# Optimization experiments

Measured on AMD Instinct MI355X. Metric: run time of the kernel, lower is better.

Reference implementation:

```python
import jax, jax.numpy as jnp
import numpy as np

P = 50000      # number of graph nodes (cortical dipoles)
HID = 256      # hidden width
E = 800000     # number of nonzeros in Ahat (avg degree 16)


def setup_inputs() -> dict:
    key = jax.random.key(0)
    ks = jax.random.split(key, 12)
    beta = jax.random.normal(ks[0], (P, 1), dtype=jnp.float32)
    degree = jax.random.uniform(ks[1], (P, 1), dtype=jnp.float32)
    A_rows = jax.random.randint(ks[2], (E,), 0, P, dtype=jnp.int32)
    A_cols = jax.random.randint(ks[3], (E,), 0, P, dtype=jnp.int32)
    # normalized-adjacency-like positive values
    A_vals = jax.random.uniform(ks[4], (E,), dtype=jnp.float32) * (1.0 / 16.0)
    # parameters (torch nn.Linear stores weight as [out, in])
    s_in = 1.0 / np.sqrt(3.0)
    s_h = 1.0 / np.sqrt(HID)
    W_in = jax.random.uniform(ks[5], (HID, 3), jnp.float32, -s_in, s_in)
    b_in = jax.random.uniform(ks[6], (HID,), jnp.float32, -s_in, s_in)
    W_mp1 = jax.random.uniform(ks[7], (HID, HID), jnp.float32, -s_h, s_h)
    W_mp2 = jax.random.uniform(ks[8], (HID, HID), jnp.float32, -s_h, s_h)
    W_out = jax.random.uniform(ks[9], (1, HID), jnp.float32, -s_h, s_h)
    b_out = jax.random.uniform(ks[10], (1,), jnp.float32, -s_h, s_h)
    return {
        "beta": beta, "degree": degree,
        "A_rows": A_rows, "A_cols": A_cols, "A_vals": A_vals,
        "W_in": W_in, "b_in": b_in,
        "W_mp1": W_mp1, "W_mp2": W_mp2,
        "W_out": W_out, "b_out": b_out,
    }


def _spmm(A_rows, A_cols, A_vals, X):
    # sparse [P,P] @ dense [P,H] via gather + segment-sum over COO edges
    msgs = A_vals[:, None] * X[A_cols]            # [E, H]
    return jax.ops.segment_sum(msgs, A_rows, num_segments=P)


def reference(beta, degree, A_rows, A_cols, A_vals,
              W_in, b_in, W_mp1, W_mp2, W_out, b_out):
    x = jnp.concatenate([beta, beta ** 2, degree], axis=1)   # [P, 3]
    h = jax.nn.relu(x @ W_in.T + b_in)                       # [P, HID]
    AH = _spmm(A_rows, A_cols, A_vals, h)                    # one-hop
    A2H = _spmm(A_rows, A_cols, A_vals, AH)                  # two-hop
    h = jax.nn.relu(AH @ W_mp1.T + A2H @ W_mp2.T)            # fused sum + relu
    g = jax.nn.softplus(h @ W_out.T + b_out)                 # [P, 1]
    return g
```

## Files before the change

kernel.cpp:

```cpp
#include <hip/hip_runtime.h>
#include <math.h>

#define NP 50000
#define HIDDEN 256
#define NE 800000
#define CAP 64

#define NSLICE 8
#define SLICE_ROWS 6250
#define BPS 256

#define OFF_AH     0ULL
#define OFF_A2H    25600000ULL
#define OFF_BP     51200000ULL
#define OFF_CNT    51462144ULL
#define OFF_PC     51662144ULL
#define OFF_EV     52062144ULL

typedef __attribute__((ext_vector_type(8))) short bf16x8;
typedef __attribute__((ext_vector_type(8))) unsigned short u16x8;
typedef __attribute__((ext_vector_type(4))) float f32x4;

__device__ inline unsigned short f2bf(float f) {
    union { float f; unsigned int u; } x; x.f = f;
    unsigned int r = x.u + 0x7FFFu + ((x.u >> 16) & 1u);
    return (unsigned short)(r >> 16);
}
__device__ inline float bf2f(unsigned short u) {
    union { unsigned int u; float f; } x; x.u = ((unsigned int)u) << 16; return x.f;
}

__global__ void bp_kernel(const float* __restrict__ W1,
                          const float* __restrict__ W2,
                          unsigned short* __restrict__ Bp) {
    int t = blockIdx.x * 256 + threadIdx.x;
    int j = t >> 9;
    int k = t & 511;
    float v = (k < 256) ? W1[j * 256 + k] : W2[j * 256 + (k - 256)];
    Bp[(k >> 3) * 2048 + j * 8 + (k & 7)] = f2bf(v);
}

__global__ void pc_kernel(const float* __restrict__ beta,
                          const float* __restrict__ degree,
                          float2* __restrict__ pc) {
    int i = blockIdx.x * 256 + threadIdx.x;
    if (i < NP) pc[i] = make_float2(beta[i], degree[i]);
}

__global__ __launch_bounds__(256) void scatter_sliced(
        const int* __restrict__ rows, const int* __restrict__ cols,
        const float* __restrict__ vals,
        int* __restrict__ cnt, int2* __restrict__ ev) {
    int slice = blockIdx.x & (NSLICE - 1);
    int bj = blockIdx.x >> 3;
    int rlo = slice * SLICE_ROWS;
    int rhi = rlo + SLICE_ROWS;
    for (int e = bj * 256 + threadIdx.x; e < NE; e += BPS * 256) {
        int r = rows[e];
        if (r >= rlo && r < rhi) {
            int pos = atomicAdd(&cnt[r], 1);
            if (pos < CAP)
                ev[(size_t)r * CAP + pos] = make_int2(cols[e], __float_as_int(vals[e]));
        }
    }
}

__global__ __launch_bounds__(256) void spmm_embed_kernel(
        const int* __restrict__ cnt, const int2* __restrict__ ev,
        const float2* __restrict__ pc,
        const float* __restrict__ W_in, const float* __restrict__ b_in,
        unsigned short* __restrict__ Y) {
    int w = threadIdx.x >> 6;
    int lane = threadIdx.x & 63;
    int r = blockIdx.x * 4 + w;
    if (r >= NP) return;
    int half = lane >> 5;
    int fo = (lane & 31) * 8;

    int n = min(cnt[r], CAP);
    int2 e2 = make_int2(0, 0);
    if (lane < n) e2 = ev[(size_t)r * CAP + lane];
    int col_l = e2.x;
    float val_l = __int_as_float(e2.y);

    float wr0[8], wr1[8], wr2[8], br[8];
    #pragma unroll
    for (int j = 0; j < 8; ++j) {
        wr0[j] = W_in[(fo + j) * 3 + 0];
        wr1[j] = W_in[(fo + j) * 3 + 1];
        wr2[j] = W_in[(fo + j) * 3 + 2];
        br[j]  = b_in[fo + j];
    }

    float acc[8] = {0.f,0.f,0.f,0.f,0.f,0.f,0.f,0.f};

#define ESTEP(d)                                                             \
    {                                                                        \
        float2 pr[d]; float vr[d];                                           \
        _Pragma("unroll")                                                    \
        for (int k = 0; k < (d); ++k) {                                      \
            int e = i + 2 * k + half;                                        \
            int c = __shfl(col_l, e);                                        \
            vr[k] = __shfl(val_l, e);                                        \
            pr[k] = pc[c];                                                   \
        }                                                                    \
        _Pragma("unroll")                                                    \
        for (int k = 0; k < (d); ++k) {                                      \
            float b = pr[k].x, dd = pr[k].y, v = vr[k];                      \
            float b2 = b * b;                                                \
            _Pragma("unroll")                                                \
            for (int j = 0; j < 8; ++j) {                                    \
                float t = fmaf(b, wr0[j], fmaf(b2, wr1[j], fmaf(dd, wr2[j], br[j]))); \
                acc[j] = fmaf(v, fmaxf(t, 0.f), acc[j]);                     \
            }                                                                \
        }                                                                    \
    }

    int i = 0;
    for (; i + 16 <= n; i += 16) ESTEP(8)
    if (i + 8 <= n) { ESTEP(4) i += 8; }
    if (i + 4 <= n) { ESTEP(2) i += 4; }
    if (i < n)      { ESTEP(2) }
#undef ESTEP

    #pragma unroll
    for (int j = 0; j < 8; ++j) acc[j] += __shfl_xor(acc[j], 32);
    if (half == 0) {
        u16x8 o;
        #pragma unroll
        for (int j = 0; j < 8; ++j) o[j] = f2bf(acc[j]);
        *reinterpret_cast<u16x8*>(Y + (size_t)r * HIDDEN + fo) = o;
    }
}

__global__ __launch_bounds__(256) void spmm_gather_kernel(
        const int* __restrict__ cnt, const int2* __restrict__ ev,
        const unsigned short* __restrict__ X,
        unsigned short* __restrict__ Y) {
    int w = threadIdx.x >> 6;
    int lane = threadIdx.x & 63;
    int r = blockIdx.x * 4 + w;
    if (r >= NP) return;
    int half = lane >> 5;
    int fo = (lane & 31) * 8;

    int n = min(cnt[r], CAP);
    int2 e2 = make_int2(0, 0);
    if (lane < n) e2 = ev[(size_t)r * CAP + lane];
    int col_l = e2.x;
    float val_l = __int_as_float(e2.y);

    float acc[8] = {0.f,0.f,0.f,0.f,0.f,0.f,0.f,0.f};

#define GSTEP(d)                                                             \
    {                                                                        \
        u16x8 xr[d]; float vr[d];                                            \
        _Pragma("unroll")                                                    \
        for (int k = 0; k < (d); ++k) {                                      \
            int e = i + 2 * k + half;                                        \
            int c = __shfl(col_l, e);                                        \
            vr[k] = __shfl(val_l, e);                                        \
            xr[k] = *reinterpret_cast<const u16x8*>(X + (size_t)c * HIDDEN + fo); \
        }                                                                    \
        _Pragma("unroll")                                                    \
        for (int k = 0; k < (d); ++k)                                        \
            _Pragma("unroll")                                                \
            for (int j = 0; j < 8; ++j)                                      \
                acc[j] = fmaf(vr[k], bf2f(xr[k][j]), acc[j]);                \
    }

    int i = 0;
    for (; i + 16 <= n; i += 16) GSTEP(8)
    if (i + 8 <= n) { GSTEP(4) i += 8; }
    if (i + 4 <= n) { GSTEP(2) i += 4; }
    if (i < n)      { GSTEP(2) }
#undef GSTEP

    #pragma unroll
    for (int j = 0; j < 8; ++j) acc[j] += __shfl_xor(acc[j], 32);
    if (half == 0) {
        u16x8 o;
        #pragma unroll
        for (int j = 0; j < 8; ++j) o[j] = f2bf(acc[j]);
        *reinterpret_cast<u16x8*>(Y + (size_t)r * HIDDEN + fo) = o;
    }
}

__global__ __launch_bounds__(512, 4) void mp_out_kernel(
        const unsigned short* __restrict__ AH,
        const unsigned short* __restrict__ A2H,
        const unsigned short* __restrict__ Bp,
        const float* __restrict__ W_out, const float* __restrict__ b_out,
        float* __restrict__ g) {
    __shared__ unsigned short As[128 * 64];
    __shared__ unsigned short Bs[8 * 256 * 8];
    __shared__ float Ps[4][128];

    int tid = threadIdx.x;
    int w = tid >> 6;
    int lane = tid & 63;
    int wr = w >> 2;
    int wc = w & 3;
    int p0 = blockIdx.x * 128;

    f32x4 acc[4][4];
    #pragma unroll
    for (int i = 0; i < 4; ++i)
        #pragma unroll
        for (int j = 0; j < 4; ++j)
            acc[i][j] = (f32x4){0.f, 0.f, 0.f, 0.f};

    for (int kc = 0; kc < 8; ++kc) {
        const unsigned short* Xsrc = (kc < 4) ? AH : A2H;
        int k0 = (kc & 3) * 64;
        __syncthreads();
        #pragma unroll
        for (int it = 0; it < 2; ++it) {
            int slot = it * 512 + tid;
            int ss = slot ^ ((slot >> 3) & 7);
            int row = ss >> 3;
            int ko = (ss & 7) * 8;
            int grow = p0 + row;
            if (grow >= NP) grow = NP - 1;
            float4 v = *reinterpret_cast<const float4*>(Xsrc + (size_t)grow * HIDDEN + k0 + ko);
            *reinterpret_cast<float4*>(&As[slot * 8]) = v;
        }
        #pragma unroll
        for (int it = 0; it < 4; ++it) {
            int c2 = it * 512 + tid;
            float4 v = *reinterpret_cast<const float4*>(
                Bp + ((size_t)(kc * 8 + (c2 >> 8))) * 2048 + (c2 & 255) * 8);
            *reinterpret_cast<float4*>(&Bs[c2 * 8]) = v;
        }
        __syncthreads();
        #pragma unroll
        for (int ks = 0; ks < 2; ++ks) {
            bf16x8 af[4], bfr[4];
            #pragma unroll
            for (int rt = 0; rt < 4; ++rt) {
                int row = wr * 64 + rt * 16 + (lane & 15);
                int elem = row * 64 + ks * 32 + (lane >> 4) * 8;
                elem ^= (row & 7) << 3;
                af[rt] = *reinterpret_cast<const bf16x8*>(&As[elem]);
            }
            #pragma unroll
            for (int nt = 0; nt < 4; ++nt) {
                int col = wc * 64 + nt * 16 + (lane & 15);
                int kbl = ks * 4 + (lane >> 4);
                bfr[nt] = *reinterpret_cast<const bf16x8*>(&Bs[kbl * 2048 + col * 8]);
            }
            #pragma unroll
            for (int rt = 0; rt < 4; ++rt)
                #pragma unroll
                for (int nt = 0; nt < 4; ++nt)
                    acc[rt][nt] = __builtin_amdgcn_mfma_f32_16x16x32_bf16(
                        af[rt], bfr[nt], acc[rt][nt], 0, 0, 0);
        }
    }

    float wv[4];
    #pragma unroll
    for (int nt = 0; nt < 4; ++nt)
        wv[nt] = W_out[wc * 64 + nt * 16 + (lane & 15)];

    float ps[4][4];
    #pragma unroll
    for (int rt = 0; rt < 4; ++rt)
        #pragma unroll
        for (int r = 0; r < 4; ++r) {
            float s = 0.f;
            #pragma unroll
            for (int nt = 0; nt < 4; ++nt)
                s = fmaf(fmaxf(acc[rt][nt][r], 0.0f), wv[nt], s);
            ps[rt][r] = s;
        }
    #pragma unroll
    for (int m = 1; m < 16; m <<= 1)
        #pragma unroll
        for (int rt = 0; rt < 4; ++rt)
            #pragma unroll
            for (int r = 0; r < 4; ++r)
                ps[rt][r] += __shfl_xor(ps[rt][r], m);

    if ((lane & 15) == 0) {
        int rb = wr * 64 + (lane >> 4) * 4;
        #pragma unroll
        for (int rt = 0; rt < 4; ++rt)
            #pragma unroll
            for (int r = 0; r < 4; ++r)
                Ps[wc][rb + rt * 16 + r] = ps[rt][r];
    }
    __syncthreads();
    if (tid < 128) {
        int p = p0 + tid;
        if (p < NP) {
            float z = Ps[0][tid] + Ps[1][tid] + Ps[2][tid] + Ps[3][tid] + b_out[0];
            g[p] = fmaxf(z, 0.0f) + log1pf(expf(-fabsf(z)));
        }
    }
}

extern "C" void kernel_launch(void* const* d_in, const int* in_sizes, int n_in,
                              void* d_out, int out_size, void* d_ws, size_t ws_size,
                              hipStream_t stream) {
    const float* beta   = (const float*)d_in[0];
    const float* degree = (const float*)d_in[1];
    const int*   A_rows = (const int*)d_in[2];
    const int*   A_cols = (const int*)d_in[3];
    const float* A_vals = (const float*)d_in[4];
    const float* W_in   = (const float*)d_in[5];
    const float* b_in   = (const float*)d_in[6];
    const float* W_mp1  = (const float*)d_in[7];
    const float* W_mp2  = (const float*)d_in[8];
    const float* W_out  = (const float*)d_in[9];
    const float* b_out  = (const float*)d_in[10];
    float* g = (float*)d_out;

    char* ws = (char*)d_ws;
    unsigned short* AH  = (unsigned short*)(ws + OFF_AH);
    unsigned short* A2H = (unsigned short*)(ws + OFF_A2H);
    unsigned short* Bp  = (unsigned short*)(ws + OFF_BP);
    int*    cnt = (int*)(ws + OFF_CNT);
    float2* pc  = (float2*)(ws + OFF_PC);
    int2*   ev  = (int2*)(ws + OFF_EV);

    hipMemsetAsync(cnt, 0, NP * sizeof(int), stream);

    bp_kernel<<<512, 256, 0, stream>>>(W_mp1, W_mp2, Bp);
    pc_kernel<<<(NP + 255) / 256, 256, 0, stream>>>(beta, degree, pc);

    scatter_sliced<<<NSLICE * BPS, 256, 0, stream>>>(A_rows, A_cols, A_vals, cnt, ev);

    spmm_embed_kernel<<<(NP + 3) / 4, 256, 0, stream>>>(cnt, ev, pc, W_in, b_in, AH);
    spmm_gather_kernel<<<(NP + 3) / 4, 256, 0, stream>>>(cnt, ev, AH, A2H);

    mp_out_kernel<<<(NP + 127) / 128, 512, 0, stream>>>(AH, A2H, Bp, W_out, b_out, g);
}
```

Before: 171.1 us.

## Use persistent waves with edge-list prefetch in SpMM kernels; fuse prep kernels

The two SpMM kernels become persistent: a grid of 2048 blocks whose waves loop over rows with a stride, prefetching the next row's count and edge list while the current row is processed. The variable-depth unrolled steps are replaced by a fixed 4-pair step plus one masked tail step. The weight repack, the beta/degree packing and the counter memset are merged into one prep kernel to cut launch overhead. In exchange, each wave holds fewer gathers in flight per step, which could reduce memory-level parallelism. The unmasked read of ev past the count also reads stale workspace entries, which are only consumed through masked lanes.

```diff
diff --git a/kernel.cpp b/kernel.cpp
--- a/kernel.cpp
+++ b/kernel.cpp
@@ -9,6 +9,9 @@
 #define NSLICE 8
 #define SLICE_ROWS 6250
 #define BPS 256
+
+#define PWB 2048
+#define PWAVES (PWB * 4)
 
 #define OFF_AH     0ULL
 #define OFF_A2H    25600000ULL
@@ -30,21 +33,27 @@
     union { unsigned int u; float f; } x; x.u = ((unsigned int)u) << 16; return x.f;
 }
 
-__global__ void bp_kernel(const float* __restrict__ W1,
-                          const float* __restrict__ W2,
-                          unsigned short* __restrict__ Bp) {
-    int t = blockIdx.x * 256 + threadIdx.x;
-    int j = t >> 9;
-    int k = t & 511;
-    float v = (k < 256) ? W1[j * 256 + k] : W2[j * 256 + (k - 256)];
-    Bp[(k >> 3) * 2048 + j * 8 + (k & 7)] = f2bf(v);
-}
-
-__global__ void pc_kernel(const float* __restrict__ beta,
-                          const float* __restrict__ degree,
-                          float2* __restrict__ pc) {
-    int i = blockIdx.x * 256 + threadIdx.x;
-    if (i < NP) pc[i] = make_float2(beta[i], degree[i]);
+__global__ void prep_kernel(const float* __restrict__ W1,
+                            const float* __restrict__ W2,
+                            unsigned short* __restrict__ Bp,
+                            const float* __restrict__ beta,
+                            const float* __restrict__ degree,
+                            float2* __restrict__ pc,
+                            int* __restrict__ cnt) {
+    int b = blockIdx.x;
+    if (b < 512) {
+        int t = b * 256 + threadIdx.x;
+        int j = t >> 9;
+        int k = t & 511;
+        float v = (k < 256) ? W1[j * 256 + k] : W2[j * 256 + (k - 256)];
+        Bp[(k >> 3) * 2048 + j * 8 + (k & 7)] = f2bf(v);
+    } else if (b < 708) {
+        int i = (b - 512) * 256 + threadIdx.x;
+        if (i < NP) pc[i] = make_float2(beta[i], degree[i]);
+    } else {
+        int i = (b - 708) * 256 + threadIdx.x;
+        if (i < NP) cnt[i] = 0;
+    }
 }
 
 __global__ __launch_bounds__(256) void scatter_sliced(
@@ -72,16 +81,8 @@
         unsigned short* __restrict__ Y) {
     int w = threadIdx.x >> 6;
     int lane = threadIdx.x & 63;
-    int r = blockIdx.x * 4 + w;
-    if (r >= NP) return;
     int half = lane >> 5;
     int fo = (lane & 31) * 8;
-
-    int n = min(cnt[r], CAP);
-    int2 e2 = make_int2(0, 0);
-    if (lane < n) e2 = ev[(size_t)r * CAP + lane];
-    int col_l = e2.x;
-    float val_l = __int_as_float(e2.y);
 
     float wr0[8], wr1[8], wr2[8], br[8];
     #pragma unroll
@@ -92,20 +93,40 @@
         br[j]  = b_in[fo + j];
     }
 
-    float acc[8] = {0.f,0.f,0.f,0.f,0.f,0.f,0.f,0.f};
-
-#define ESTEP(d)                                                             \
+    int r = blockIdx.x * 4 + w;
+    if (r >= NP) return;
+    int  n_cur = cnt[r];
+    int2 e_cur = ev[(size_t)r * CAP + lane];
+
+    while (true) {
+        int rn = r + PWAVES;
+        int  n_nxt = 0;
+        int2 e_nxt = make_int2(0, 0);
+        if (rn < NP) {
+            n_nxt = cnt[rn];
+            e_nxt = ev[(size_t)rn * CAP + lane];
+        }
+
+        int n = min(n_cur, CAP);
+        int col_l = e_cur.x;
+        float val_l = __int_as_float(e_cur.y);
+        float acc[8] = {0.f,0.f,0.f,0.f,0.f,0.f,0.f,0.f};
+
+#define ESTEP(MASKED)                                                        \
     {                                                                        \
-        float2 pr[d]; float vr[d];                                           \
+        float2 pr[4]; float vr[4];                                           \
         _Pragma("unroll")                                                    \
-        for (int k = 0; k < (d); ++k) {                                      \
+        for (int k = 0; k < 4; ++k) {                                        \
             int e = i + 2 * k + half;                                        \
-            int c = __shfl(col_l, e);                                        \
-            vr[k] = __shfl(val_l, e);                                        \
+            int es = (MASKED) ? ((e < n) ? e : 0) : e;                       \
+            int c = __shfl(col_l, es);                                       \
+            float vt = __shfl(val_l, es);                                    \
+            if (MASKED) vt = (e < n) ? vt : 0.f;                             \
+            vr[k] = vt;                                                      \
             pr[k] = pc[c];                                                   \
         }                                                                    \
         _Pragma("unroll")                                                    \
-        for (int k = 0; k < (d); ++k) {                                      \
+        for (int k = 0; k < 4; ++k) {                                        \
             float b = pr[k].x, dd = pr[k].y, v = vr[k];                      \
             float b2 = b * b;                                                \
             _Pragma("unroll")                                                \
@@ -116,20 +137,22 @@
         }                                                                    \
     }
 
-    int i = 0;
-    for (; i + 16 <= n; i += 16) ESTEP(8)
-    if (i + 8 <= n) { ESTEP(4) i += 8; }
-    if (i + 4 <= n) { ESTEP(2) i += 4; }
-    if (i < n)      { ESTEP(2) }
+        int i = 0;
+        for (; i + 8 <= n; i += 8) ESTEP(false)
+        if (i < n) ESTEP(true)
 #undef ESTEP
 
-    #pragma unroll
-    for (int j = 0; j < 8; ++j) acc[j] += __shfl_xor(acc[j], 32);
-    if (half == 0) {
-        u16x8 o;
-        #pragma unroll
-        for (int j = 0; j < 8; ++j) o[j] = f2bf(acc[j]);
-        *reinterpret_cast<u16x8*>(Y + (size_t)r * HIDDEN + fo) = o;
+        #pragma unroll
+        for (int j = 0; j < 8; ++j) acc[j] += __shfl_xor(acc[j], 32);
+        if (half == 0) {
+            u16x8 o;
+            #pragma unroll
+            for (int j = 0; j < 8; ++j) o[j] = f2bf(acc[j]);
+            *reinterpret_cast<u16x8*>(Y + (size_t)r * HIDDEN + fo) = o;
+        }
+
+        if (rn >= NP) break;
+        r = rn; n_cur = n_nxt; e_cur = e_nxt;
     }
 }
 
@@ -139,50 +162,64 @@
         unsigned short* __restrict__ Y) {
     int w = threadIdx.x >> 6;
     int lane = threadIdx.x & 63;
+    int half = lane >> 5;
+    int fo = (lane & 31) * 8;
+
     int r = blockIdx.x * 4 + w;
     if (r >= NP) return;
-    int half = lane >> 5;
-    int fo = (lane & 31) * 8;
-
-    int n = min(cnt[r], CAP);
-    int2 e2 = make_int2(0, 0);
-    if (lane < n) e2 = ev[(size_t)r * CAP + lane];
-    int col_l = e2.x;
-    float val_l = __int_as_float(e2.y);
-
-    float acc[8] = {0.f,0.f,0.f,0.f,0.f,0.f,0.f,0.f};
-
-#define GSTEP(d)                                                             \
+    int  n_cur = cnt[r];
+    int2 e_cur = ev[(size_t)r * CAP + lane];
+
+    while (true) {
+        int rn = r + PWAVES;
+        int  n_nxt = 0;
+        int2 e_nxt = make_int2(0, 0);
+        if (rn < NP) {
+            n_nxt = cnt[rn];
+            e_nxt = ev[(size_t)rn * CAP + lane];
+        }
+
+        int n = min(n_cur, CAP);
+        int col_l = e_cur.x;
+        float val_l = __int_as_float(e_cur.y);
+        float acc[8] = {0.f,0.f,0.f,0.f,0.f,0.f,0.f,0.f};
+
+#define GSTEP(MASKED)                                                        \
     {                                                                        \
-        u16x8 xr[d]; float vr[d];                                            \
+        u16x8 xr[4]; float vr[4];                                            \
         _Pragma("unroll")                                                    \
-        for (int k = 0; k < (d); ++k) {                                      \
+        for (int k = 0; k < 4; ++k) {                                        \
             int e = i + 2 * k + half;                                        \
-            int c = __shfl(col_l, e);                                        \
-            vr[k] = __shfl(val_l, e);                                        \
+            int es = (MASKED) ? ((e < n) ? e : 0) : e;                       \
+            int c = __shfl(col_l, es);                                       \
+            float vt = __shfl(val_l, es);                                    \
+            if (MASKED) vt = (e < n) ? vt : 0.f;                             \
+            vr[k] = vt;                                                      \
             xr[k] = *reinterpret_cast<const u16x8*>(X + (size_t)c * HIDDEN + fo); \
         }                                                                    \
         _Pragma("unroll")                                                    \
-        for (int k = 0; k < (d); ++k)                                        \
+        for (int k = 0; k < 4; ++k)                                          \
             _Pragma("unroll")                                                \
             for (int j = 0; j < 8; ++j)                                      \
                 acc[j] = fmaf(vr[k], bf2f(xr[k][j]), acc[j]);                \
     }
 
-    int i = 0;
-    for (; i + 16 <= n; i += 16) GSTEP(8)
-    if (i + 8 <= n) { GSTEP(4) i += 8; }
-    if (i + 4 <= n) { GSTEP(2) i += 4; }
-    if (i < n)      { GSTEP(2) }
+        int i = 0;
+        for (; i + 8 <= n; i += 8) GSTEP(false)
+        if (i < n) GSTEP(true)
 #undef GSTEP
 
-    #pragma unroll
-    for (int j = 0; j < 8; ++j) acc[j] += __shfl_xor(acc[j], 32);
-    if (half == 0) {
-        u16x8 o;
-        #pragma unroll
-        for (int j = 0; j < 8; ++j) o[j] = f2bf(acc[j]);
-        *reinterpret_cast<u16x8*>(Y + (size_t)r * HIDDEN + fo) = o;
+        #pragma unroll
+        for (int j = 0; j < 8; ++j) acc[j] += __shfl_xor(acc[j], 32);
+        if (half == 0) {
+            u16x8 o;
+            #pragma unroll
+            for (int j = 0; j < 8; ++j) o[j] = f2bf(acc[j]);
+            *reinterpret_cast<u16x8*>(Y + (size_t)r * HIDDEN + fo) = o;
+        }
+
+        if (rn >= NP) break;
+        r = rn; n_cur = n_nxt; e_cur = e_nxt;
     }
 }
 
@@ -324,15 +361,12 @@
     float2* pc  = (float2*)(ws + OFF_PC);
     int2*   ev  = (int2*)(ws + OFF_EV);
 
-    hipMemsetAsync(cnt, 0, NP * sizeof(int), stream);
-
-    bp_kernel<<<512, 256, 0, stream>>>(W_mp1, W_mp2, Bp);
-    pc_kernel<<<(NP + 255) / 256, 256, 0, stream>>>(beta, degree, pc);
+    prep_kernel<<<904, 256, 0, stream>>>(W_mp1, W_mp2, Bp, beta, degree, pc, cnt);
 
     scatter_sliced<<<NSLICE * BPS, 256, 0, stream>>>(A_rows, A_cols, A_vals, cnt, ev);
 
-    spmm_embed_kernel<<<(NP + 3) / 4, 256, 0, stream>>>(cnt, ev, pc, W_in, b_in, AH);
-    spmm_gather_kernel<<<(NP + 3) / 4, 256, 0, stream>>>(cnt, ev, AH, A2H);
+    spmm_embed_kernel<<<PWB, 256, 0, stream>>>(cnt, ev, pc, W_in, b_in, AH);
+    spmm_gather_kernel<<<PWB, 256, 0, stream>>>(cnt, ev, AH, A2H);
 
     mp_out_kernel<<<(NP + 127) / 128, 512, 0, stream>>>(AH, A2H, Bp, W_out, b_out, g);
 }
```

New measurement: 177.4 us. 1.04x slower.
